# Optimization experiments

Measured on AMD Instinct MI355X. Metric: run time of the kernel, lower is better.

The kernel has to match this reference:

```python
import jax, jax.numpy as jnp
import numpy as np

C = 256
D = C // 8  # 32


def setup_inputs() -> dict:
    key = jax.random.key(0)
    ks = jax.random.split(key, 9)
    B, H, W = 4, 64, 64
    x = jax.random.normal(ks[0], (B, C, H, W), dtype=jnp.float32)
    # 1x1 conv weights stored as [out, in] matrices (kernel_size=1)
    s = 1.0 / np.sqrt(C)
    Wf = jax.random.uniform(ks[1], (D, C), jnp.float32, -s, s)
    Wg = jax.random.uniform(ks[2], (D, C), jnp.float32, -s, s)
    Wh = jax.random.uniform(ks[3], (D, C), jnp.float32, -s, s)
    sv = 1.0 / np.sqrt(D)
    Wv = jax.random.uniform(ks[4], (C, D), jnp.float32, -sv, sv)
    bf = jnp.zeros((D,), jnp.float32)
    bg = jnp.zeros((D,), jnp.float32)
    bh = jnp.zeros((D,), jnp.float32)
    bv = jax.random.uniform(ks[5], (C,), jnp.float32, -sv, sv)
    # gamma initialized to zero in the module; use a nonzero value so output is non-trivial
    gamma = jnp.array([0.5], jnp.float32)
    return {"x": x, "Wf": Wf, "bf": bf, "Wg": Wg, "bg": bg,
            "Wh": Wh, "bh": bh, "Wv": Wv, "bv": bv, "gamma": gamma}


def reference(x, Wf, bf, Wg, bg, Wh, bh, Wv, bv, gamma):
    B, Cc, Hh, Ww = x.shape
    N = Hh * Ww
    xf = x.reshape(B, Cc, N)  # flatten spatial tokens, [B, C, N]
    # 1x1 convs == channel matmuls
    f = jnp.einsum('dc,bcn->bdn', Wf, xf) + bf[None, :, None]  # [B, D, N]
    g = jnp.einsum('dc,bcn->bdn', Wg, xf) + bg[None, :, None]
    h = jnp.einsum('dc,bcn->bdn', Wh, xf) + bh[None, :, None]
    # unscaled attention: f^T g -> [B, N, N], softmax over last axis
    attn = jax.nn.softmax(jnp.einsum('bdn,bdm->bnm', f, g), axis=-1)
    # h @ attn: out[:, d, m] = sum_n h[:, d, n] * attn[:, n, m]
    sa = jnp.einsum('bdn,bnm->bdm', h, attn)  # [B, D, N]
    # output 1x1 conv D -> C
    o = jnp.einsum('cd,bdn->bcn', Wv, sa) + bv[None, :, None]
    out = gamma[0] * o.reshape(B, Cc, Hh, Ww)
    return out
```

## Files before the change

kernel.cpp:

```cpp
#include <hip/hip_runtime.h>

typedef __bf16 bf16;
typedef bf16 bf16x4 __attribute__((ext_vector_type(4)));
typedef bf16 bf16x8 __attribute__((ext_vector_type(8)));
typedef float f32x4 __attribute__((ext_vector_type(4)));

#define NB 4
#define NC 256
#define ND 32
#define NN 4096
#define NSPLIT 4
#define MSPLIT 4

__global__ __launch_bounds__(256) void k_wcvt(
    const float* __restrict__ Wf, const float* __restrict__ Wg,
    const float* __restrict__ Wh, bf16* __restrict__ Wstk)
{
    int e0 = (blockIdx.x * 256 + threadIdx.x) * 8;
    int row = e0 >> 8;
    int tensor = row >> 5;
    const float* src = tensor == 0 ? Wf : tensor == 1 ? Wg : Wh;
    const float* sp = src + (row & 31) * NC + (e0 & 255);
    bf16x8 v;
    #pragma unroll
    for (int j = 0; j < 8; ++j) v[j] = (bf16)sp[j];
    *reinterpret_cast<bf16x8*>(Wstk + e0) = v;
}

__global__ __launch_bounds__(512) void k_fgh(
    const float* __restrict__ x,
    const bf16* __restrict__ Wstk,
    const float* __restrict__ bfp, const float* __restrict__ bgp,
    const float* __restrict__ bhp,
    bf16* __restrict__ fT, bf16* __restrict__ gT, bf16* __restrict__ hM)
{
    __shared__ __align__(16) char xb[64 * 512];
    const int b  = blockIdx.y;
    const int n0 = blockIdx.x * 64;
    const int t  = threadIdx.x;
    const int lane = t & 63;
    const int w  = t >> 6;
    const int l15 = lane & 15;
    const int l4  = lane >> 4;

    {
        const int nl  = t & 63;
        const int swz = (nl & 7) << 4;
        const int chi = (t >> 6) * 8;
        #pragma unroll
        for (int pass = 0; pass < 4; ++pass) {
            int c0 = pass * 64 + chi;
            const float* xp = x + ((size_t)b * NC + c0) * NN + n0 + nl;
            bf16x8 v;
            #pragma unroll
            for (int j = 0; j < 8; ++j) v[j] = (bf16)xp[(size_t)j * NN];
            *reinterpret_cast<bf16x8*>(&xb[nl * 512 + ((c0 * 2) ^ swz)]) = v;
        }
    }
    __syncthreads();

    const int ncol = (w & 3) * 16 + l15;
    const int nswz = (ncol & 7) << 4;
    const int n    = n0 + ncol;
    const int dsub = l4 * 4;
    const int rtb  = (w >> 2) * 3;

    #pragma unroll
    for (int rr = 0; rr < 3; ++rr) {
        int rt = rtb + rr;
        int tensor = rt >> 1;
        int d0 = (rt & 1) * 16;
        f32x4 acc = {0.f, 0.f, 0.f, 0.f};
        #pragma unroll
        for (int kc = 0; kc < 8; ++kc) {
            bf16x8 a = *reinterpret_cast<const bf16x8*>(
                Wstk + (rt * 16 + l15) * NC + kc * 32 + l4 * 8);
            bf16x8 bb = *reinterpret_cast<const bf16x8*>(
                &xb[ncol * 512 + ((kc * 64 + l4 * 16) ^ nswz)]);
            acc = __builtin_amdgcn_mfma_f32_16x16x32_bf16(a, bb, acc, 0, 0, 0);
        }
        const float* bsel = tensor == 0 ? bfp : tensor == 1 ? bgp : bhp;
        int dbase = d0 + dsub;
        if (tensor < 2) {
            bf16x4 vv;
            #pragma unroll
            for (int r = 0; r < 4; ++r) vv[r] = (bf16)(acc[r] + bsel[dbase + r]);
            bf16* dst = (tensor == 0 ? fT : gT) + ((size_t)b * NN + n) * ND + dbase;
            *reinterpret_cast<bf16x4*>(dst) = vv;
        } else {
            #pragma unroll
            for (int r = 0; r < 4; ++r)
                hM[((size_t)b * ND + dbase + r) * NN + n] =
                    (bf16)(acc[r] + bsel[dbase + r]);
        }
    }
}

__global__ __launch_bounds__(256) void k_rowsum(
    const bf16* __restrict__ fT, const bf16* __restrict__ gT,
    float* __restrict__ Lpart)
{
    const int b  = blockIdx.z;
    const int ms = blockIdx.y;
    const int nb = blockIdx.x * 64;
    const int t  = threadIdx.x;
    const int lane = t & 63;
    const int w  = t >> 6;
    const int l15 = lane & 15;
    const int l4  = lane >> 4;

    bf16x8 a = *reinterpret_cast<const bf16x8*>(
        fT + ((size_t)b * NN + nb + w * 16 + l15) * ND + l4 * 8);
    float sum0 = 0.f, sum1 = 0.f, sum2 = 0.f, sum3 = 0.f;
    const bf16* gp = gT + (size_t)b * NN * ND
                   + ((size_t)ms * (NN / MSPLIT) + l15) * ND + l4 * 8;
    #pragma unroll 4
    for (int m = 0; m < NN / MSPLIT; m += 32) {
        bf16x8 b0 = *reinterpret_cast<const bf16x8*>(gp + (size_t)m * ND);
        bf16x8 b1 = *reinterpret_cast<const bf16x8*>(gp + (size_t)(m + 16) * ND);
        f32x4 z = {0.f, 0.f, 0.f, 0.f};
        f32x4 s0 = __builtin_amdgcn_mfma_f32_16x16x32_bf16(a, b0, z, 0, 0, 0);
        f32x4 s1 = __builtin_amdgcn_mfma_f32_16x16x32_bf16(a, b1, z, 0, 0, 0);
        sum0 += __expf(s0[0]) + __expf(s1[0]);
        sum1 += __expf(s0[1]) + __expf(s1[1]);
        sum2 += __expf(s0[2]) + __expf(s1[2]);
        sum3 += __expf(s0[3]) + __expf(s1[3]);
    }
    float sv[4] = {sum0, sum1, sum2, sum3};
    #pragma unroll
    for (int r = 0; r < 4; ++r) {
        float v = sv[r];
        v += __shfl_xor(v, 1);
        v += __shfl_xor(v, 2);
        v += __shfl_xor(v, 4);
        v += __shfl_xor(v, 8);
        sv[r] = v;
    }
    if (l15 == 0) {
        #pragma unroll
        for (int r = 0; r < 4; ++r)
            Lpart[((size_t)ms * NB + b) * NN + nb + w * 16 + l4 * 4 + r] = sv[r];
    }
}

__global__ __launch_bounds__(256) void k_scaleh(
    const float* __restrict__ Lpart, bf16* __restrict__ hM)
{
    __shared__ float rls[64];
    const int b  = blockIdx.y;
    const int nb = blockIdx.x * 64;
    const int t  = threadIdx.x;
    if (t < 64) {
        float s = 0.f;
        #pragma unroll
        for (int ms = 0; ms < MSPLIT; ++ms)
            s += Lpart[((size_t)ms * NB + b) * NN + nb + t];
        rls[t] = 1.0f / s;
    }
    __syncthreads();
    int d  = t >> 3;
    int ne = (t & 7) * 8;
    bf16* hp = hM + ((size_t)b * ND + d) * NN + nb + ne;
    bf16x8 hv = *reinterpret_cast<const bf16x8*>(hp);
    bf16x8 ho;
    #pragma unroll
    for (int j = 0; j < 8; ++j) ho[j] = (bf16)((float)hv[j] * rls[ne + j]);
    *reinterpret_cast<bf16x8*>(hp) = ho;
}

__global__ __launch_bounds__(256) void k_attn(
    const bf16* __restrict__ fT, const bf16* __restrict__ gT,
    const bf16* __restrict__ hM, float* __restrict__ saWS)
{
    __shared__ __align__(16) char fL[64 * 80];
    __shared__ __align__(16) char hL[32 * 144];
    __shared__ __align__(16) char Pl[4 * 2048];

    const int b  = blockIdx.z;
    const int ns = blockIdx.y;
    const int m0 = blockIdx.x * 64;
    const int t  = threadIdx.x;
    const int lane = t & 63;
    const int w  = t >> 6;
    const int l15 = lane & 15;
    const int l4  = lane >> 4;

    bf16x8 gfrag = *reinterpret_cast<const bf16x8*>(
        gT + ((size_t)b * NN + m0 + w * 16 + l15) * ND + l4 * 8);

    f32x4 acc0 = {0.f, 0.f, 0.f, 0.f};
    f32x4 acc1 = {0.f, 0.f, 0.f, 0.f};

    char* Pw = &Pl[w * 2048];
    const int mswz = (l15 & 7) << 4;

    const int s_nl = t >> 2;
    const int s_dl = (t & 3) * 8;
    const int s_d  = t >> 3;
    const int s_ne = (t & 7) * 8;
    const bf16* fsrc = fT + (size_t)b * NN * ND;
    const bf16* hsrc = hM + (size_t)b * ND * NN;

    const int nbeg = ns * (NN / NSPLIT);
    const int nend = nbeg + NN / NSPLIT;

    for (int n1 = nbeg; n1 < nend; n1 += 64) {
        __syncthreads();
        *reinterpret_cast<bf16x8*>(&fL[s_nl * 80 + s_dl * 2]) =
            *reinterpret_cast<const bf16x8*>(fsrc + (size_t)(n1 + s_nl) * ND + s_dl);
        *reinterpret_cast<bf16x8*>(&hL[s_d * 144 + s_ne * 2]) =
            *reinterpret_cast<const bf16x8*>(hsrc + (size_t)s_d * NN + n1 + s_ne);
        __syncthreads();

        #pragma unroll
        for (int nt = 0; nt < 4; ++nt) {
            bf16x8 afrag = *reinterpret_cast<const bf16x8*>(
                &fL[(nt * 16 + l15) * 80 + l4 * 16]);
            f32x4 z = {0.f, 0.f, 0.f, 0.f};
            f32x4 s = __builtin_amdgcn_mfma_f32_16x16x32_bf16(afrag, gfrag, z, 0, 0, 0);
            bf16x4 p4;
            #pragma unroll
            for (int r = 0; r < 4; ++r) p4[r] = (bf16)__expf(s[r]);
            *reinterpret_cast<bf16x4*>(
                &Pw[l15 * 128 + ((nt * 32 + l4 * 8) ^ mswz)]) = p4;
        }
        #pragma unroll
        for (int kc = 0; kc < 2; ++kc) {
            bf16x8 pb = *reinterpret_cast<const bf16x8*>(
                &Pw[l15 * 128 + ((kc * 64 + l4 * 16) ^ mswz)]);
            bf16x8 h0 = *reinterpret_cast<const bf16x8*>(
                &hL[l15 * 144 + kc * 64 + l4 * 16]);
            acc0 = __builtin_amdgcn_mfma_f32_16x16x32_bf16(h0, pb, acc0, 0, 0, 0);
            bf16x8 h1 = *reinterpret_cast<const bf16x8*>(
                &hL[(16 + l15) * 144 + kc * 64 + l4 * 16]);
            acc1 = __builtin_amdgcn_mfma_f32_16x16x32_bf16(h1, pb, acc1, 0, 0, 0);
        }
    }

    float* sp = saWS + (((size_t)ns * NB + b) * NN + m0 + w * 16 + l15) * ND;
    *reinterpret_cast<f32x4*>(sp + l4 * 4)      = acc0;
    *reinterpret_cast<f32x4*>(sp + 16 + l4 * 4) = acc1;
}

__global__ __launch_bounds__(1024) void k_proj(
    const float* __restrict__ saWS,
    const float* __restrict__ Wv, const float* __restrict__ bv,
    const float* __restrict__ gamma, float* __restrict__ out)
{
    __shared__ float sa_s[64 * 33];
    const int b  = blockIdx.y;
    const int m0 = blockIdx.x * 64;
    const int t  = threadIdx.x;

    #pragma unroll
    for (int p = t; p < 64 * 32; p += 1024) {
        int m = p >> 5, d = p & 31;
        float s = 0.f;
        #pragma unroll
        for (int s4 = 0; s4 < NSPLIT; ++s4)
            s += saWS[(((size_t)s4 * NB + b) * NN + m0 + m) * ND + d];
        sa_s[m * 33 + d] = s;
    }
    __syncthreads();

    const int mloc = t & 63;
    const int cg   = t >> 6;
    float sav[32];
    #pragma unroll
    for (int d = 0; d < 32; ++d) sav[d] = sa_s[mloc * 33 + d];
    const float g0 = gamma[0];
    float* op = out + (size_t)b * NC * NN + m0 + mloc;
    #pragma unroll
    for (int i = 0; i < 16; ++i) {
        int c = cg * 16 + i;
        const float* wp = Wv + c * ND;
        float sum = bv[c];
        #pragma unroll
        for (int d = 0; d < 32; ++d) sum = fmaf(wp[d], sav[d], sum);
        op[(size_t)c * NN] = g0 * sum;
    }
}

extern "C" void kernel_launch(void* const* d_in, const int* in_sizes, int n_in,
                              void* d_out, int out_size, void* d_ws, size_t ws_size,
                              hipStream_t stream)
{
    const float* x   = (const float*)d_in[0];
    const float* Wf  = (const float*)d_in[1];
    const float* bfp = (const float*)d_in[2];
    const float* Wg  = (const float*)d_in[3];
    const float* bgp = (const float*)d_in[4];
    const float* Wh  = (const float*)d_in[5];
    const float* bhp = (const float*)d_in[6];
    const float* Wv  = (const float*)d_in[7];
    const float* bv  = (const float*)d_in[8];
    const float* gm  = (const float*)d_in[9];
    float* out = (float*)d_out;

    char* ws = (char*)d_ws;
    bf16*  Wstk  = (bf16*)ws;
    bf16*  fT    = (bf16*)(ws + 49152);
    bf16*  gT    = (bf16*)(ws + 49152 + (1u << 20));
    bf16*  hM    = (bf16*)(ws + 49152 + (2u << 20));
    float* Lpart = (float*)(ws + 49152 + (3u << 20));
    float* saWS  = (float*)(ws + 49152 + (3u << 20) + (256u << 10));

    k_wcvt  <<<dim3(12),              dim3(256),  0, stream>>>(Wf, Wg, Wh, Wstk);
    k_fgh   <<<dim3(64, NB),          dim3(512),  0, stream>>>(x, Wstk, bfp, bgp, bhp, fT, gT, hM);
    k_rowsum<<<dim3(64, MSPLIT, NB),  dim3(256),  0, stream>>>(fT, gT, Lpart);
    k_scaleh<<<dim3(64, NB),          dim3(256),  0, stream>>>(Lpart, hM);
    k_attn  <<<dim3(64, NSPLIT, NB),  dim3(256),  0, stream>>>(fT, gT, hM, saWS);
    k_proj  <<<dim3(64, NB),          dim3(1024), 0, stream>>>(saWS, Wv, bv, gm, out);
}
```

Measured before the change: 157.1 us.

## Fuse row-normalization into attention, double split counts, split projection over channels

```diff
diff --git a/kernel.cpp b/kernel.cpp
--- a/kernel.cpp
+++ b/kernel.cpp
@@ -9,8 +9,9 @@
 #define NC 256
 #define ND 32
 #define NN 4096
-#define NSPLIT 4
-#define MSPLIT 4
+#define NSPLIT 8
+#define MSPLIT 8
+#define CSPL 8
 
 __global__ __launch_bounds__(256) void k_wcvt(
     const float* __restrict__ Wf, const float* __restrict__ Wg,
@@ -143,38 +144,15 @@
     }
 }
 
-__global__ __launch_bounds__(256) void k_scaleh(
-    const float* __restrict__ Lpart, bf16* __restrict__ hM)
-{
-    __shared__ float rls[64];
-    const int b  = blockIdx.y;
-    const int nb = blockIdx.x * 64;
-    const int t  = threadIdx.x;
-    if (t < 64) {
-        float s = 0.f;
-        #pragma unroll
-        for (int ms = 0; ms < MSPLIT; ++ms)
-            s += Lpart[((size_t)ms * NB + b) * NN + nb + t];
-        rls[t] = 1.0f / s;
-    }
-    __syncthreads();
-    int d  = t >> 3;
-    int ne = (t & 7) * 8;
-    bf16* hp = hM + ((size_t)b * ND + d) * NN + nb + ne;
-    bf16x8 hv = *reinterpret_cast<const bf16x8*>(hp);
-    bf16x8 ho;
-    #pragma unroll
-    for (int j = 0; j < 8; ++j) ho[j] = (bf16)((float)hv[j] * rls[ne + j]);
-    *reinterpret_cast<bf16x8*>(hp) = ho;
-}
-
 __global__ __launch_bounds__(256) void k_attn(
     const bf16* __restrict__ fT, const bf16* __restrict__ gT,
-    const bf16* __restrict__ hM, float* __restrict__ saWS)
+    const bf16* __restrict__ hM, const float* __restrict__ Lpart,
+    float* __restrict__ saWS)
 {
     __shared__ __align__(16) char fL[64 * 80];
     __shared__ __align__(16) char hL[32 * 144];
     __shared__ __align__(16) char Pl[4 * 2048];
+    __shared__ float rlL[64];
 
     const int b  = blockIdx.z;
     const int ns = blockIdx.y;
@@ -210,6 +188,13 @@
             *reinterpret_cast<const bf16x8*>(fsrc + (size_t)(n1 + s_nl) * ND + s_dl);
         *reinterpret_cast<bf16x8*>(&hL[s_d * 144 + s_ne * 2]) =
             *reinterpret_cast<const bf16x8*>(hsrc + (size_t)s_d * NN + n1 + s_ne);
+        if (t < 64) {
+            float s = 0.f;
+            #pragma unroll
+            for (int ms = 0; ms < MSPLIT; ++ms)
+                s += Lpart[((size_t)ms * NB + b) * NN + n1 + t];
+            rlL[t] = 1.0f / s;
+        }
         __syncthreads();
 
         #pragma unroll
@@ -220,7 +205,8 @@
             f32x4 s = __builtin_amdgcn_mfma_f32_16x16x32_bf16(afrag, gfrag, z, 0, 0, 0);
             bf16x4 p4;
             #pragma unroll
-            for (int r = 0; r < 4; ++r) p4[r] = (bf16)__expf(s[r]);
+            for (int r = 0; r < 4; ++r)
+                p4[r] = (bf16)(__expf(s[r]) * rlL[nt * 16 + l4 * 4 + r]);
             *reinterpret_cast<bf16x4*>(
                 &Pw[l15 * 128 + ((nt * 32 + l4 * 8) ^ mswz)]) = p4;
         }
@@ -242,24 +228,29 @@
     *reinterpret_cast<f32x4*>(sp + 16 + l4 * 4) = acc1;
 }
 
-__global__ __launch_bounds__(1024) void k_proj(
+__global__ __launch_bounds__(256) void k_proj(
     const float* __restrict__ saWS,
     const float* __restrict__ Wv, const float* __restrict__ bv,
     const float* __restrict__ gamma, float* __restrict__ out)
 {
     __shared__ float sa_s[64 * 33];
-    const int b  = blockIdx.y;
+    const int b  = blockIdx.z;
+    const int c0 = blockIdx.y * (NC / CSPL);
     const int m0 = blockIdx.x * 64;
     const int t  = threadIdx.x;
 
     #pragma unroll
-    for (int p = t; p < 64 * 32; p += 1024) {
-        int m = p >> 5, d = p & 31;
-        float s = 0.f;
-        #pragma unroll
-        for (int s4 = 0; s4 < NSPLIT; ++s4)
-            s += saWS[(((size_t)s4 * NB + b) * NN + m0 + m) * ND + d];
-        sa_s[m * 33 + d] = s;
+    for (int p = t; p < 64 * 8; p += 256) {
+        int m = p >> 3, dq = (p & 7) * 4;
+        float s0 = 0.f, s1 = 0.f, s2 = 0.f, s3 = 0.f;
+        #pragma unroll
+        for (int s4 = 0; s4 < NSPLIT; ++s4) {
+            f32x4 v = *reinterpret_cast<const f32x4*>(
+                saWS + (((size_t)s4 * NB + b) * NN + m0 + m) * ND + dq);
+            s0 += v[0]; s1 += v[1]; s2 += v[2]; s3 += v[3];
+        }
+        float* dp = &sa_s[m * 33 + dq];
+        dp[0] = s0; dp[1] = s1; dp[2] = s2; dp[3] = s3;
     }
     __syncthreads();
 
@@ -271,8 +262,8 @@
     const float g0 = gamma[0];
     float* op = out + (size_t)b * NC * NN + m0 + mloc;
     #pragma unroll
-    for (int i = 0; i < 16; ++i) {
-        int c = cg * 16 + i;
+    for (int i = 0; i < 8; ++i) {
+        int c = c0 + cg * 8 + i;
         const float* wp = Wv + c * ND;
         float sum = bv[c];
         #pragma unroll
@@ -303,12 +294,11 @@
     bf16*  gT    = (bf16*)(ws + 49152 + (1u << 20));
     bf16*  hM    = (bf16*)(ws + 49152 + (2u << 20));
     float* Lpart = (float*)(ws + 49152 + (3u << 20));
-    float* saWS  = (float*)(ws + 49152 + (3u << 20) + (256u << 10));
-
-    k_wcvt  <<<dim3(12),              dim3(256),  0, stream>>>(Wf, Wg, Wh, Wstk);
-    k_fgh   <<<dim3(64, NB),          dim3(512),  0, stream>>>(x, Wstk, bfp, bgp, bhp, fT, gT, hM);
-    k_rowsum<<<dim3(64, MSPLIT, NB),  dim3(256),  0, stream>>>(fT, gT, Lpart);
-    k_scaleh<<<dim3(64, NB),          dim3(256),  0, stream>>>(Lpart, hM);
-    k_attn  <<<dim3(64, NSPLIT, NB),  dim3(256),  0, stream>>>(fT, gT, hM, saWS);
-    k_proj  <<<dim3(64, NB),          dim3(1024), 0, stream>>>(saWS, Wv, bv, gm, out);
-}
+    float* saWS  = (float*)(ws + 49152 + (3u << 20) + (512u << 10));
+
+    k_wcvt  <<<dim3(12),              dim3(256), 0, stream>>>(Wf, Wg, Wh, Wstk);
+    k_fgh   <<<dim3(64, NB),          dim3(512), 0, stream>>>(x, Wstk, bfp, bgp, bhp, fT, gT, hM);
+    k_rowsum<<<dim3(64, MSPLIT, NB),  dim3(256), 0, stream>>>(fT, gT, Lpart);
+    k_attn  <<<dim3(64, NSPLIT, NB),  dim3(256), 0, stream>>>(fT, gT, hM, Lpart, saWS);
+    k_proj  <<<dim3(64, CSPL, NB),    dim3(256), 0, stream>>>(saWS, Wv, bv, gm, out);
+}
```

Result: no change. 157.3 us (+0.2%).
